# Kernel optimization log

Hardware: AMD Instinct MI355X
Metric: run time of the kernel (lower is better)

Reference implementation:

```python
import jax, jax.numpy as jnp
import numpy as np

H, F = 4, 32          # GAT heads, per-head channels (= hidden_dim)
NEG_ATT = 0.2         # GATConv attention leaky_relu slope (PyG default)
NEG_ACT = 0.01        # F.leaky_relu / nn.LeakyReLU default slope
NUM_ID = 9            # len(map_candid_to_numid)


def _leaky(x, s):
    return jnp.where(x >= 0, x, s * x)


def gat_conv(x, src, dst, n, W, att_src, att_dst, bias):
    # PyG GATConv(heads=4, concat=False): softmax over in-edges per dst node,
    # weighted scatter-add, mean over heads, then bias.
    h = (x @ W).reshape(n, H, F)
    a_s = jnp.einsum('nhf,hf->nh', h, att_src)
    a_d = jnp.einsum('nhf,hf->nh', h, att_dst)
    e = _leaky(a_s[src] + a_d[dst], NEG_ATT)                        # [E,H]
    m = jax.ops.segment_max(e, dst, num_segments=n)                 # stable softmax max
    m = jnp.where(jnp.isfinite(m), m, 0.0)
    ex = jnp.exp(e - m[dst])
    denom = jax.ops.segment_sum(ex, dst, num_segments=n) + 1e-16    # PyG softmax eps
    alpha = ex / denom[dst]
    out = jax.ops.segment_sum(alpha[:, :, None] * h[src], dst, num_segments=n)
    return out.mean(axis=1) + bias


def _gat_params(k, din):
    k1, k2, k3 = jax.random.split(k, 3)
    return (jax.random.normal(k1, (din, H * F), jnp.float32) * np.float32(1.0 / np.sqrt(din)),
            jax.random.normal(k2, (H, F), jnp.float32) * 0.1,
            jax.random.normal(k3, (H, F), jnp.float32) * 0.1,
            jnp.zeros((F,), jnp.float32))


def setup_inputs() -> dict:
    key = jax.random.key(0)
    ks = jax.random.split(key, 20)
    N, E, D = 100000, 800000, 3
    x = jax.random.normal(ks[0], (N, D), jnp.float32)
    x = x.at[: N // 2, 0].set(0.0)  # towers: x[:,0] == 0
    edge_index = jax.random.randint(ks[1], (2, E), 0, N, dtype=jnp.int64)
    edge_attr = jax.random.uniform(ks[2], (E, 1), dtype=jnp.float32)
    inp = {'x': x, 'edge_index': edge_index, 'edge_attr': edge_attr}
    for i, din in enumerate([D, F, F]):
        W, a_s, a_d, b = _gat_params(ks[3 + i], din)
        inp[f'W{i+1}'] = W; inp[f'a_src{i+1}'] = a_s
        inp[f'a_dst{i+1}'] = a_d; inp[f'b{i+1}'] = b
    mlp_dims = [(D + F, F), (F, F), (F, F), (F, F), (F, NUM_ID + 3)]
    for i, (di, do) in enumerate(mlp_dims):
        k1, k2 = jax.random.split(ks[10 + i])
        inp[f'mW{i+1}'] = jax.random.normal(k1, (di, do), jnp.float32) * np.float32(1.0 / np.sqrt(di))
        inp[f'mb{i+1}'] = jax.random.normal(k2, (do,), jnp.float32) * 0.01
    return inp


def reference(x, edge_index, edge_attr, W1, a_src1, a_dst1, b1,
              W2, a_src2, a_dst2, b2, W3, a_src3, a_dst3, b3,
              mW1, mb1, mW2, mb2, mW3, mb3, mW4, mb4, mW5, mb5):
    # edge_attr / batch are read but unused by the torch forward.
    n = x.shape[0]
    loops = jnp.arange(n, dtype=edge_index.dtype)  # add_self_loops=True
    src = jnp.concatenate([edge_index[0], loops])
    dst = jnp.concatenate([edge_index[1], loops])
    x1 = _leaky(gat_conv(x, src, dst, n, W1, a_src1, a_dst1, b1), NEG_ACT)
    x2 = _leaky(gat_conv(x1, src, dst, n, W2, a_src2, a_dst2, b2), NEG_ACT)
    x3 = _leaky(gat_conv(x2, src, dst, n, W3, a_src3, a_dst3, b3), NEG_ACT)
    h = jnp.concatenate([x, x3], axis=-1)
    for W, b in [(mW1, mb1), (mW2, mb2), (mW3, mb3), (mW4, mb4)]:
        h = _leaky(h @ W + b, NEG_ACT)  # Dropout(0.5) is identity in eval
    cands = h @ mW5 + mb5               # [N, 12]
    mask_tower = x[:, 0] == 0           # data-dependent split (eager-mode indexing)
    ct = cands[mask_tower]
    ck = cands[~mask_tower]
    return (ct[:, :NUM_ID], ck[:, :NUM_ID], ct[:, NUM_ID:], ck[:, NUM_ID:])
```

## Files before the change

kernel.cpp:

```cpp
#include <hip/hip_runtime.h>
#include <hip/hip_bf16.h>

#define DEV __device__ __forceinline__

DEV float bf2f(__hip_bfloat16 v) { return __bfloat162float(v); }

typedef unsigned long long ull;

__global__ void k_detect_zero(const unsigned short* xr, int nprobe, int* flag,
                              int* cnt, int N) {
    int i = blockIdx.x * 256 + threadIdx.x;
    if (i < N) cnt[i] = 0;
    if (blockIdx.x == 0) {
        __shared__ int red[256];
        int t = threadIdx.x, bad = 0;
        for (int j = t; j < nprobe; j += 256) {
            unsigned e = (xr[j] >> 7) & 0xFF;
            if (e >= 0x8F) bad++;
        }
        red[t] = bad; __syncthreads();
        for (int o = 128; o > 0; o >>= 1) { if (t < o) red[t] += red[t + o]; __syncthreads(); }
        if (t == 0) flag[0] = (red[0] > 256) ? 1 : 0;
    }
}

struct Seg  { const void* src; int off; int len; };
struct Segs { Seg s[22]; };

__global__ void k_fused(const void* xsrc, int nx3, Segs segs, float* canon,
                        const int* flag, const int* eidx, int E, int N,
                        int* cnt, int* msk, int* rank) {
    int f32 = flag[0];
    int t = threadIdx.x, b = blockIdx.x;
    if (b < 64) {
        for (int i = b * 256 + t; i < nx3; i += 64 * 256) {
            float v = f32 ? ((const float*)xsrc)[i] : bf2f(((const __hip_bfloat16*)xsrc)[i]);
            if (!(v == v) || fabsf(v) > 1e30f) v = 0.f;
            canon[i] = v;
            if (i % 3 == 0) msk[i / 3] = (v == 0.0f) ? 1 : 0;
        }
    } else if (b < 86) {
        Seg sg = segs.s[b - 64];
        for (int i = t; i < sg.len; i += 256) {
            float v = f32 ? ((const float*)sg.src)[i] : bf2f(((const __hip_bfloat16*)sg.src)[i]);
            if (!(v == v) || fabsf(v) > 1e30f) v = 0.f;
            canon[sg.off + i] = v;
        }
    } else {
        int e = (b - 86) * 256 + t;
        if (e < E) {
            int d = eidx[E + e];
            if ((unsigned)d < (unsigned)N) {
                int p = atomicAdd(&cnt[d], 1);
                rank[e] = p;
            }
        }
    }
}


DEV ull packval(const int* cnt, const int* msk, int i) {
    return ((ull)(unsigned)msk[i] << 32) | (unsigned)(cnt[i] + 1);
}

__global__ void k_scan_partial64(const int* __restrict__ cnt, const int* __restrict__ msk,
                                 int n, ull* __restrict__ partials) {
    __shared__ ull red[256];
    int t = threadIdx.x, b = blockIdx.x;
    int base = b * 1024 + t * 4;
    ull s = 0;
    #pragma unroll
    for (int j = 0; j < 4; j++) { int i = base + j; if (i < n) s += packval(cnt, msk, i); }
    red[t] = s; __syncthreads();
    for (int o = 128; o > 0; o >>= 1) { if (t < o) red[t] += red[t + o]; __syncthreads(); }
    if (t == 0) partials[b] = red[0];
}

__global__ void k_scan_final64(const int* __restrict__ cnt, int* __restrict__ msk, int n,
                               const ull* __restrict__ partials, int nb,
                               int* __restrict__ off, int* __restrict__ offN,
                               int* __restrict__ totals) {
    __shared__ ull sums[256];
    __shared__ ull redLT[256], redALL[256];
    int t = threadIdx.x, b = blockIdx.x;

    ull sLT = 0, sALL = 0;
    for (int i = t; i < nb; i += 256) {
        ull v = partials[i];
        sALL += v;
        if (i < b) sLT += v;
    }
    redLT[t] = sLT; redALL[t] = sALL; __syncthreads();
    for (int o = 128; o > 0; o >>= 1) {
        if (t < o) { redLT[t] += redLT[t + o]; redALL[t] += redALL[t + o]; }
        __syncthreads();
    }
    ull blockbase = redLT[0];
    if (b == 0 && t == 0) {
        ull tot = redALL[0];
        *offN = (int)(tot & 0xffffffffu);
        *totals = (int)(tot >> 32);
    }
    __syncthreads();

    int base = b * 1024 + t * 4;
    ull v0 = 0, v1 = 0, v2 = 0, v3 = 0;
    if (base     < n) v0 = packval(cnt, msk, base);
    if (base + 1 < n) v1 = packval(cnt, msk, base + 1);
    if (base + 2 < n) v2 = packval(cnt, msk, base + 2);
    if (base + 3 < n) v3 = packval(cnt, msk, base + 3);
    ull s = v0 + v1 + v2 + v3;
    sums[t] = s; __syncthreads();
    for (int o = 1; o < 256; o <<= 1) {
        ull x = (t >= o) ? sums[t - o] : 0;
        __syncthreads();
        sums[t] += x;
        __syncthreads();
    }
    ull run = blockbase + (sums[t] - s);
    #pragma unroll
    for (int j = 0; j < 4; j++) {
        int i = base + j;
        if (i < n) {
            off[i] = (int)(run & 0xffffffffu);
            msk[i] = (int)(run >> 32);
            run += (j == 0 ? v0 : j == 1 ? v1 : j == 2 ? v2 : v3);
        }
    }
}


__global__ __launch_bounds__(256) void k_fill_node1(
    const int* __restrict__ eidx, const int* __restrict__ rank, int E, int N,
    const int* __restrict__ off, int* __restrict__ esrc,
    const float* __restrict__ xF, const float* __restrict__ W,
    const float* __restrict__ atS, const float* __restrict__ atD,
    __hip_bfloat162* __restrict__ h2, float* __restrict__ as_, float* __restrict__ ad_,
    int gfill) {
    __shared__ float xl[64 * 4];
    int b = blockIdx.x;
    if (b < gfill) {
        int e = b * 256 + threadIdx.x;
        if (e < E) {
            int s = eidx[e], d = eidx[E + e];
            if ((unsigned)d < (unsigned)N && (unsigned)s < (unsigned)N)
                esrc[off[d] + rank[e]] = s;
        } else if (e < E + N) {
            int i = e - E;
            esrc[off[i + 1] - 1] = i;
        }
        return;
    }
    int t = threadIdx.x, lane = t & 63, w = t >> 6;
    int nblk = (b - gfill) * 64;
    int cnt = N - nblk; if (cnt > 64) cnt = 64;

    if (t < 64) xl[t * 4 + 3] = 0.f;
    for (int i = t; i < cnt * 3; i += 256) xl[(i / 3) * 4 + (i % 3)] = xF[(size_t)nblk * 3 + i];

    const float2* W2 = (const float2*)W;
    float2 Wr0 = W2[0 * 64 + lane], Wr1 = W2[1 * 64 + lane], Wr2 = W2[2 * 64 + lane];
    float2 aSp = ((const float2*)atS)[lane];
    float2 aDp = ((const float2*)atD)[lane];
    int hd = lane >> 4;
    __syncthreads();

    for (int i = 0; i < 16; i++) {
        int n = nblk + w * 16 + i;
        if (n >= N) break;
        float4 xv = ((const float4*)xl)[w * 16 + i];
        float acc0 = xv.x * Wr0.x + xv.y * Wr1.x + xv.z * Wr2.x;
        float acc1 = xv.x * Wr0.y + xv.y * Wr1.y + xv.z * Wr2.y;
        __hip_bfloat162 hv; hv.x = __float2bfloat16(acc0); hv.y = __float2bfloat16(acc1);
        h2[(size_t)n * 64 + lane] = hv;
        float p = acc0 * aSp.x + acc1 * aSp.y;
        float q = acc0 * aDp.x + acc1 * aDp.y;
        #pragma unroll
        for (int o = 1; o < 16; o <<= 1) { p += __shfl_xor(p, o, 64); q += __shfl_xor(q, o, 64); }
        if ((lane & 15) == 0) { as_[n * 4 + hd] = p; ad_[n * 4 + hd] = q; }
    }
}


__global__ __launch_bounds__(256) void k_node_mid(
    const float* __restrict__ xin, const float* __restrict__ W,
    const float* __restrict__ atS, const float* __restrict__ atD,
    int N, __hip_bfloat162* __restrict__ h2, float* __restrict__ as_, float* __restrict__ ad_) {
    __shared__ float xl[64 * 32];
    int t = threadIdx.x, lane = t & 63, w = t >> 6;
    int nblk = blockIdx.x * 64;
    int cnt = N - nblk; if (cnt > 64) cnt = 64;

    {
        const float4* g4 = (const float4*)(xin + (size_t)nblk * 32);
        float4* l4 = (float4*)xl;
        int lim = cnt * 8;
        if (t < lim) l4[t] = g4[t];
        int t2 = t + 256;
        if (t2 < lim) l4[t2] = g4[t2];
    }

    const float2* W2 = (const float2*)W;
    float2 Wr[32];
    #pragma unroll
    for (int k = 0; k < 32; k++) Wr[k] = W2[k * 64 + lane];
    float2 aSp = ((const float2*)atS)[lane];
    float2 aDp = ((const float2*)atD)[lane];
    int hd = lane >> 4;
    __syncthreads();

    for (int i = 0; i < 16; i++) {
        int n = nblk + w * 16 + i;
        if (n >= N) break;
        const float4* xv4 = (const float4*)&xl[(w * 16 + i) * 32];
        float acc0 = 0.f, acc1 = 0.f;
        #pragma unroll
        for (int kk = 0; kk < 8; kk++) {
            float4 xv = xv4[kk];
            acc0 += xv.x * Wr[4*kk+0].x; acc1 += xv.x * Wr[4*kk+0].y;
            acc0 += xv.y * Wr[4*kk+1].x; acc1 += xv.y * Wr[4*kk+1].y;
            acc0 += xv.z * Wr[4*kk+2].x; acc1 += xv.z * Wr[4*kk+2].y;
            acc0 += xv.w * Wr[4*kk+3].x; acc1 += xv.w * Wr[4*kk+3].y;
        }
        __hip_bfloat162 hv; hv.x = __float2bfloat16(acc0); hv.y = __float2bfloat16(acc1);
        h2[(size_t)n * 64 + lane] = hv;
        float p = acc0 * aSp.x + acc1 * aSp.y;
        float q = acc0 * aDp.x + acc1 * aDp.y;
        #pragma unroll
        for (int o = 1; o < 16; o <<= 1) { p += __shfl_xor(p, o, 64); q += __shfl_xor(q, o, 64); }
        if ((lane & 15) == 0) { as_[n * 4 + hd] = p; ad_[n * 4 + hd] = q; }
    }
}


constexpr int FCAP  = 64;
constexpr int FCAPP = 68;

__global__ __launch_bounds__(256) void k_edge(
    const __hip_bfloat162* __restrict__ h2, const float* __restrict__ as_,
    const float* __restrict__ ad_, const int* __restrict__ off,
    const int* __restrict__ esrc, const float* __restrict__ bias,
    int N, float* __restrict__ xout) {
    __shared__ float alphaS[4][4 * FCAPP];
    __shared__ int   srcS[4][FCAP];
    int t = threadIdx.x, lane = t & 63, w = t >> 6;
    int n = blockIdx.x * 4 + w;
    if (n >= N) return;
    int beg = off[n], end = off[n + 1];
    int deg = end - beg;
    float4 adn = ((const float4*)ad_)[n];
    const float4* as4 = (const float4*)as_;
    int hd = lane >> 4;

    float acc0 = 0.f, acc1 = 0.f;

    if (deg <= 16) {
        int e = lane >> 2, h = lane & 3;
        int s_e = n;
        float v = -1e30f;
        if (e < deg) {
            int s = esrc[beg + e];
            if ((unsigned)s < (unsigned)N) {
                s_e = s;
                float asv = as_[s * 4 + h];
                float adv = h == 0 ? adn.x : h == 1 ? adn.y : h == 2 ? adn.z : adn.w;
                v = asv + adv; v = v >= 0.f ? v : 0.2f * v;
            }
        }
        float m = v;
        #pragma unroll
        for (int o = 4; o < 64; o <<= 1) m = fmaxf(m, __shfl_xor(m, o, 64));
        float ex = (v > -1e29f) ? __expf(v - m) : 0.f;
        float ssum = ex;
        #pragma unroll
        for (int o = 4; o < 64; o <<= 1) ssum += __shfl_xor(ssum, o, 64);
        float inv = 1.f / (ssum + 1e-16f);
        float invH = __shfl(inv, hd, 64);

        #pragma unroll
        for (int c = 0; c < 4; c++) {
            if (4 * c < deg) {
                float w0 = __shfl(ex, 16 * c + 0  + hd, 64);
                float w1 = __shfl(ex, 16 * c + 4  + hd, 64);
                float w2 = __shfl(ex, 16 * c + 8  + hd, 64);
                float w3 = __shfl(ex, 16 * c + 12 + hd, 64);
                int s0 = __shfl(s_e, 16 * c + 0, 64);
                int s1 = __shfl(s_e, 16 * c + 4, 64);
                int s2 = __shfl(s_e, 16 * c + 8, 64);
                int s3 = __shfl(s_e, 16 * c + 12, 64);
                __hip_bfloat162 g0 = h2[(size_t)s0 * 64 + lane];
                __hip_bfloat162 g1 = h2[(size_t)s1 * 64 + lane];
                __hip_bfloat162 g2 = h2[(size_t)s2 * 64 + lane];
                __hip_bfloat162 g3 = h2[(size_t)s3 * 64 + lane];
                acc0 += w0 * bf2f(g0.x) + w1 * bf2f(g1.x) + w2 * bf2f(g2.x) + w3 * bf2f(g3.x);
                acc1 += w0 * bf2f(g0.y) + w1 * bf2f(g1.y) + w2 * bf2f(g2.y) + w3 * bf2f(g3.y);
            }
        }
        acc0 *= invH; acc1 *= invH;
    } else {
        bool fits = (deg <= FCAP);
        float m0 = -1e30f, m1 = -1e30f, m2 = -1e30f, m3 = -1e30f;
        for (int e = beg + lane; e < end; e += 64) {
            int s = esrc[e];
            if ((unsigned)s >= (unsigned)N) continue;
            float4 a = as4[s];
            float v0 = a.x + adn.x; v0 = v0 >= 0.f ? v0 : 0.2f * v0;
            float v1 = a.y + adn.y; v1 = v1 >= 0.f ? v1 : 0.2f * v1;
            float v2 = a.z + adn.z; v2 = v2 >= 0.f ? v2 : 0.2f * v2;
            float v3 = a.w + adn.w; v3 = v3 >= 0.f ? v3 : 0.2f * v3;
            m0 = fmaxf(m0, v0); m1 = fmaxf(m1, v1); m2 = fmaxf(m2, v2); m3 = fmaxf(m3, v3);
        }
        #pragma unroll
        for (int o = 1; o < 64; o <<= 1) {
            m0 = fmaxf(m0, __shfl_xor(m0, o, 64));
            m1 = fmaxf(m1, __shfl_xor(m1, o, 64));
            m2 = fmaxf(m2, __shfl_xor(m2, o, 64));
            m3 = fmaxf(m3, __shfl_xor(m3, o, 64));
        }
        float s0 = 0.f, s1 = 0.f, s2 = 0.f, s3 = 0.f;
        for (int e = beg + lane; e < end; e += 64) {
            int s = esrc[e];
            bool ok = (unsigned)s < (unsigned)N;
            float4 a = ok ? as4[s] : make_float4(-1e30f, -1e30f, -1e30f, -1e30f);
            float v0 = a.x + adn.x; v0 = v0 >= 0.f ? v0 : 0.2f * v0;
            float v1 = a.y + adn.y; v1 = v1 >= 0.f ? v1 : 0.2f * v1;
            float v2 = a.z + adn.z; v2 = v2 >= 0.f ? v2 : 0.2f * v2;
            float v3 = a.w + adn.w; v3 = v3 >= 0.f ? v3 : 0.2f * v3;
            float e0 = __expf(v0 - m0), e1 = __expf(v1 - m1);
            float e2 = __expf(v2 - m2), e3 = __expf(v3 - m3);
            s0 += e0; s1 += e1; s2 += e2; s3 += e3;
            if (fits) {
                int i = e - beg;
                srcS[w][i] = ok ? s : n;
                alphaS[w][0 * FCAPP + i] = e0;
                alphaS[w][1 * FCAPP + i] = e1;
                alphaS[w][2 * FCAPP + i] = e2;
                alphaS[w][3 * FCAPP + i] = e3;
            }
        }
        #pragma unroll
        for (int o = 1; o < 64; o <<= 1) {
            s0 += __shfl_xor(s0, o, 64); s1 += __shfl_xor(s1, o, 64);
            s2 += __shfl_xor(s2, o, 64); s3 += __shfl_xor(s3, o, 64);
        }
        float i0 = 1.f / (s0 + 1e-16f), i1 = 1.f / (s1 + 1e-16f);
        float i2 = 1.f / (s2 + 1e-16f), i3 = 1.f / (s3 + 1e-16f);
        float invH = hd == 0 ? i0 : hd == 1 ? i1 : hd == 2 ? i2 : i3;
        if (fits) {
            for (int i = 0; i < deg; i++) {
                int s = srcS[w][i];
                float wt = alphaS[w][hd * FCAPP + i];
                __hip_bfloat162 hv = h2[(size_t)s * 64 + lane];
                acc0 += wt * bf2f(hv.x);
                acc1 += wt * bf2f(hv.y);
            }
        } else {
            float mH  = hd == 0 ? m0 : hd == 1 ? m1 : hd == 2 ? m2 : m3;
            float adH = hd == 0 ? adn.x : hd == 1 ? adn.y : hd == 2 ? adn.z : adn.w;
            for (int e = beg; e < end; e++) {
                int s = esrc[e];
                if ((unsigned)s >= (unsigned)N) continue;
                float4 a = as4[s];
                float aH = hd == 0 ? a.x : hd == 1 ? a.y : hd == 2 ? a.z : a.w;
                float v = aH + adH; v = v >= 0.f ? v : 0.2f * v;
                float wt = __expf(v - mH);
                __hip_bfloat162 hv = h2[(size_t)s * 64 + lane];
                acc0 += wt * bf2f(hv.x);
                acc1 += wt * bf2f(hv.y);
            }
        }
        acc0 *= invH; acc1 *= invH;
    }
    acc0 += __shfl_xor(acc0, 16, 64); acc0 += __shfl_xor(acc0, 32, 64);
    acc1 += __shfl_xor(acc1, 16, 64); acc1 += __shfl_xor(acc1, 32, 64);
    if (lane < 16) {
        float o0 = acc0 * 0.25f + bias[2 * lane];     o0 = o0 >= 0.f ? o0 : 0.01f * o0;
        float o1 = acc1 * 0.25f + bias[2 * lane + 1]; o1 = o1 >= 0.f ? o1 : 0.01f * o1;
        ((float2*)xout)[(size_t)n * 16 + lane] = make_float2(o0, o1);
    }
}


__global__ __launch_bounds__(128) void k_mlp(
    const float* __restrict__ xF, const float* __restrict__ x3,
    const float* __restrict__ mW1, const float* __restrict__ mb1,
    const float* __restrict__ mW2, const float* __restrict__ mb2,
    const float* __restrict__ mW3, const float* __restrict__ mb3,
    const float* __restrict__ mW4, const float* __restrict__ mb4,
    const float* __restrict__ mW5, const float* __restrict__ mb5,
    const int* __restrict__ smask, const int* __restrict__ totals,
    const int* __restrict__ flag, int N, void* __restrict__ out) {
    __shared__ float W1[35 * 32], W2[1024], W3[1024], W4[1024], W5[32 * 12];
    __shared__ float B1[32], B2[32], B3[32], B4[32], B5[12];
    __shared__ float actA[35 * 128];
    __shared__ float actB[32 * 128];
    int t = threadIdx.x;
    for (int i = t; i < 1120; i += 128) W1[i] = mW1[i];
    for (int i = t; i < 1024; i += 128) { W2[i] = mW2[i]; W3[i] = mW3[i]; W4[i] = mW4[i]; }
    for (int i = t; i < 384; i += 128) W5[i] = mW5[i];
    if (t < 32) { B1[t] = mb1[t]; B2[t] = mb2[t]; B3[t] = mb3[t]; B4[t] = mb4[t]; }
    if (t < 12) B5[t] = mb5[t];
    __syncthreads();

    int n = blockIdx.x * 128 + t;
    bool alive = (n < N);
    float x0 = 0.f;
    if (alive) {
        x0 = xF[n * 3 + 0];
        actA[0 * 128 + t] = x0;
        actA[1 * 128 + t] = xF[n * 3 + 1];
        actA[2 * 128 + t] = xF[n * 3 + 2];
        for (int i = 0; i < 32; i++) actA[(3 + i) * 128 + t] = x3[(size_t)n * 32 + i];
    }

    float acc[32];

    #pragma unroll
    for (int o = 0; o < 32; o++) acc[o] = B1[o];
    #pragma unroll 2
    for (int i = 0; i < 35; i++) {
        float ai = actA[i * 128 + t];
        const float4* w4 = (const float4*)&W1[i * 32];
        #pragma unroll
        for (int q = 0; q < 8; q++) {
            float4 w = w4[q];
            acc[q*4+0] += ai * w.x; acc[q*4+1] += ai * w.y;
            acc[q*4+2] += ai * w.z; acc[q*4+3] += ai * w.w;
        }
    }
    #pragma unroll
    for (int o = 0; o < 32; o++) { float v = acc[o]; actB[o * 128 + t] = (v >= 0.f ? v : 0.01f * v); }

    #pragma unroll
    for (int o = 0; o < 32; o++) acc[o] = B2[o];
    #pragma unroll 2
    for (int i = 0; i < 32; i++) {
        float ai = actB[i * 128 + t];
        const float4* w4 = (const float4*)&W2[i * 32];
        #pragma unroll
        for (int q = 0; q < 8; q++) {
            float4 w = w4[q];
            acc[q*4+0] += ai * w.x; acc[q*4+1] += ai * w.y;
            acc[q*4+2] += ai * w.z; acc[q*4+3] += ai * w.w;
        }
    }
    #pragma unroll
    for (int o = 0; o < 32; o++) { float v = acc[o]; actA[o * 128 + t] = (v >= 0.f ? v : 0.01f * v); }

    #pragma unroll
    for (int o = 0; o < 32; o++) acc[o] = B3[o];
    #pragma unroll 2
    for (int i = 0; i < 32; i++) {
        float ai = actA[i * 128 + t];
        const float4* w4 = (const float4*)&W3[i * 32];
        #pragma unroll
        for (int q = 0; q < 8; q++) {
            float4 w = w4[q];
            acc[q*4+0] += ai * w.x; acc[q*4+1] += ai * w.y;
            acc[q*4+2] += ai * w.z; acc[q*4+3] += ai * w.w;
        }
    }
    #pragma unroll
    for (int o = 0; o < 32; o++) { float v = acc[o]; actB[o * 128 + t] = (v >= 0.f ? v : 0.01f * v); }

    #pragma unroll
    for (int o = 0; o < 32; o++) acc[o] = B4[o];
    #pragma unroll 2
    for (int i = 0; i < 32; i++) {
        float ai = actB[i * 128 + t];
        const float4* w4 = (const float4*)&W4[i * 32];
        #pragma unroll
        for (int q = 0; q < 8; q++) {
            float4 w = w4[q];
            acc[q*4+0] += ai * w.x; acc[q*4+1] += ai * w.y;
            acc[q*4+2] += ai * w.z; acc[q*4+3] += ai * w.w;
        }
    }
    #pragma unroll
    for (int o = 0; o < 32; o++) { float v = acc[o]; actA[o * 128 + t] = (v >= 0.f ? v : 0.01f * v); }

    float d[12];
    #pragma unroll
    for (int o = 0; o < 12; o++) d[o] = B5[o];
    #pragma unroll 2
    for (int i = 0; i < 32; i++) {
        float ai = actA[i * 128 + t];
        const float4* w4 = (const float4*)&W5[i * 12];
        #pragma unroll
        for (int q = 0; q < 3; q++) {
            float4 w = w4[q];
            d[q*4+0] += ai * w.x; d[q*4+1] += ai * w.y;
            d[q*4+2] += ai * w.z; d[q*4+3] += ai * w.w;
        }
    }
    if (!alive) return;
    #pragma unroll
    for (int o = 0; o < 12; o++) if (!(d[o] == d[o])) d[o] = 0.f;

    bool tower = (x0 == 0.0f);
    int r = smask[n];
    int Nt = *totals;
    int f32o = *flag;
    int base9, base3, rr;
    if (tower) { rr = r;     base9 = 0;      base3 = 9 * N; }
    else       { rr = n - r; base9 = 9 * Nt; base3 = 9 * N + 3 * Nt; }
    if (f32o) {
        float* o = (float*)out;
        #pragma unroll
        for (int j = 0; j < 9; j++) o[base9 + rr * 9 + j] = d[j];
        #pragma unroll
        for (int j = 0; j < 3; j++) o[base3 + rr * 3 + j] = d[9 + j];
    } else {
        __hip_bfloat16* o = (__hip_bfloat16*)out;
        #pragma unroll
        for (int j = 0; j < 9; j++) o[base9 + rr * 9 + j] = __float2bfloat16(d[j]);
        #pragma unroll
        for (int j = 0; j < 3; j++) o[base3 + rr * 3 + j] = __float2bfloat16(d[9 + j]);
    }
}


extern "C" void kernel_launch(void* const* d_in, const int* in_sizes, int n_in,
                              void* d_out, int out_size, void* d_ws, size_t ws_size,
                              hipStream_t stream) {
    const void* xraw = d_in[0];
    const int*  eidx = (const int*)d_in[1];

    int N  = in_sizes[0] / 3;
    int E  = in_sizes[1] / 2;
    int EE = E + N;

    Segs segs;
    int coff[22];
    int canonN = 3 * N;
    for (int i = 3; i <= 24; i++) {
        int a = i - 3;
        segs.s[a].src = d_in[i];
        segs.s[a].off = canonN;
        segs.s[a].len = in_sizes[i];
        coff[a] = canonN;
        canonN += in_sizes[i];
    }

    auto alignv = [](size_t v, size_t a) { return (v + a - 1) & ~(a - 1); };
    char* base = (char*)d_ws;
    size_t o = 0;
    float* canon = (float*)(base + o); o = alignv(o + (size_t)canonN * 4, 16);
    int* flag     = (int*)(base + o); o = alignv(o + 16, 16);
    ull* partials = (ull*)(base + o); o = alignv(o + 1024 * 8, 16);
    int* totals   = (int*)(base + o); o = alignv(o + 16, 16);
    int* off      = (int*)(base + o); o = alignv(o + (size_t)(N + 1) * 4, 16);
    int* cnt      = (int*)(base + o); o = alignv(o + (size_t)N * 4, 16);
    int* esrc     = (int*)(base + o); o = alignv(o + (size_t)EE * 4, 16);
    int* rank     = (int*)(base + o); o = alignv(o + (size_t)E * 4, 16);
    int* msk      = (int*)(base + o); o = alignv(o + (size_t)N * 4, 256);
    __hip_bfloat162* h2 = (__hip_bfloat162*)(base + o); o = alignv(o + (size_t)N * 64 * 4, 16);
    float* xb  = (float*)(base + o); o = alignv(o + (size_t)N * 32 * 4, 16);
    float* as_ = (float*)(base + o); o = alignv(o + (size_t)N * 16, 16);
    float* ad_ = (float*)(base + o);

    int nb = (N + 1023) / 1024;
    int gN = (N + 255) / 256;
    int g4 = (N + 3) / 4;
    int g64 = (N + 63) / 64;
    int gM = (N + 127) / 128;
    int gfill = (EE + 255) / 256;

    int nprobe = in_sizes[0] < 4096 ? in_sizes[0] : 4096;
    k_detect_zero<<<gN, 256, 0, stream>>>((const unsigned short*)xraw, nprobe, flag, cnt, N);
    k_fused<<<86 + (E + 255) / 256, 256, 0, stream>>>(xraw, 3 * N, segs, canon, flag,
                                                      eidx, E, N, cnt, msk, rank);
    k_scan_partial64<<<nb, 256, 0, stream>>>(cnt, msk, N, partials);
    k_scan_final64<<<nb, 256, 0, stream>>>(cnt, msk, N, partials, nb, off, off + N, totals);

    float* xF = canon;
    const float* W1  = canon + coff[0];  const float* aS1 = canon + coff[1];
    const float* aD1 = canon + coff[2];  const float* b1  = canon + coff[3];
    const float* W2  = canon + coff[4];  const float* aS2 = canon + coff[5];
    const float* aD2 = canon + coff[6];  const float* b2  = canon + coff[7];
    const float* W3  = canon + coff[8];  const float* aS3 = canon + coff[9];
    const float* aD3 = canon + coff[10]; const float* b3  = canon + coff[11];

    k_fill_node1<<<gfill + g64, 256, 0, stream>>>(eidx, rank, E, N, off, esrc,
                                                  xF, W1, aS1, aD1, h2, as_, ad_, gfill);
    k_edge<<<g4, 256, 0, stream>>>(h2, as_, ad_, off, esrc, b1, N, xb);
    k_node_mid<<<g64, 256, 0, stream>>>(xb, W2, aS2, aD2, N, h2, as_, ad_);
    k_edge<<<g4, 256, 0, stream>>>(h2, as_, ad_, off, esrc, b2, N, xb);
    k_node_mid<<<g64, 256, 0, stream>>>(xb, W3, aS3, aD3, N, h2, as_, ad_);
    k_edge<<<g4, 256, 0, stream>>>(h2, as_, ad_, off, esrc, b3, N, xb);

    k_mlp<<<gM, 128, 0, stream>>>(xF, xb,
        canon + coff[12], canon + coff[13], canon + coff[14], canon + coff[15],
        canon + coff[16], canon + coff[17], canon + coff[18], canon + coff[19],
        canon + coff[20], canon + coff[21], msk, totals, flag, N, d_out);
}
```

Before: 436.3 us.

## Fold dtype detection into fused prep kernel and stage edge weights in LDS

Removes the separate detection kernel. Every block of the fused prep kernel now probes the input dtype itself, and cnt is zeroed with an async memset. In the low-degree path of the edge kernel, the softmax weights and source indices go into shared memory and are read back as float4/int4 vectors instead of through many cross-lane shuffles. The cost is that every block of the large fused grid now does the redundant 4096-element probe and reduction, which adds work and global reads per block.

Measured after the change: 437.3 us. No clear change (+0.2%).

```diff
diff --git a/kernel.cpp b/kernel.cpp
--- a/kernel.cpp
+++ b/kernel.cpp
@@ -7,31 +7,25 @@
 
 typedef unsigned long long ull;
 
-__global__ void k_detect_zero(const unsigned short* xr, int nprobe, int* flag,
-                              int* cnt, int N) {
-    int i = blockIdx.x * 256 + threadIdx.x;
-    if (i < N) cnt[i] = 0;
-    if (blockIdx.x == 0) {
-        __shared__ int red[256];
-        int t = threadIdx.x, bad = 0;
-        for (int j = t; j < nprobe; j += 256) {
-            unsigned e = (xr[j] >> 7) & 0xFF;
-            if (e >= 0x8F) bad++;
-        }
-        red[t] = bad; __syncthreads();
-        for (int o = 128; o > 0; o >>= 1) { if (t < o) red[t] += red[t + o]; __syncthreads(); }
-        if (t == 0) flag[0] = (red[0] > 256) ? 1 : 0;
-    }
-}
-
 struct Seg  { const void* src; int off; int len; };
 struct Segs { Seg s[22]; };
 
-__global__ void k_fused(const void* xsrc, int nx3, Segs segs, float* canon,
-                        const int* flag, const int* eidx, int E, int N,
+__global__ void k_fused(const void* xsrc, int nx3, int nprobe, Segs segs,
+                        float* canon, int* flag, const int* eidx, int E, int N,
                         int* cnt, int* msk, int* rank) {
-    int f32 = flag[0];
+    __shared__ int red[256];
     int t = threadIdx.x, b = blockIdx.x;
+    const unsigned short* xr = (const unsigned short*)xsrc;
+    int bad = 0;
+    for (int j = t; j < nprobe; j += 256) {
+        unsigned e = (xr[j] >> 7) & 0xFF;
+        if (e >= 0x8F) bad++;
+    }
+    red[t] = bad; __syncthreads();
+    for (int o = 128; o > 0; o >>= 1) { if (t < o) red[t] += red[t + o]; __syncthreads(); }
+    int f32 = (red[0] > 256) ? 1 : 0;
+    if (b == 0 && t == 0) flag[0] = f32;
+
     if (b < 64) {
         for (int i = b * 256 + t; i < nx3; i += 64 * 256) {
             float v = f32 ? ((const float*)xsrc)[i] : bf2f(((const __hip_bfloat16*)xsrc)[i]);
@@ -241,8 +235,8 @@
     const float* __restrict__ ad_, const int* __restrict__ off,
     const int* __restrict__ esrc, const float* __restrict__ bias,
     int N, float* __restrict__ xout) {
-    __shared__ float alphaS[4][4 * FCAPP];
-    __shared__ int   srcS[4][FCAP];
+    __shared__ __align__(16) float alphaS[4][4 * FCAPP];
+    __shared__ __align__(16) int   srcS[4][FCAP];
     int t = threadIdx.x, lane = t & 63, w = t >> 6;
     int n = blockIdx.x * 4 + w;
     if (n >= N) return;
@@ -277,23 +271,22 @@
         float inv = 1.f / (ssum + 1e-16f);
         float invH = __shfl(inv, hd, 64);
 
+        alphaS[w][h * 20 + e] = ex;
+        if (h == 0) srcS[w][e] = s_e;
+
         #pragma unroll
         for (int c = 0; c < 4; c++) {
             if (4 * c < deg) {
-                float w0 = __shfl(ex, 16 * c + 0  + hd, 64);
-                float w1 = __shfl(ex, 16 * c + 4  + hd, 64);
-                float w2 = __shfl(ex, 16 * c + 8  + hd, 64);
-                float w3 = __shfl(ex, 16 * c + 12 + hd, 64);
-                int s0 = __shfl(s_e, 16 * c + 0, 64);
-                int s1 = __shfl(s_e, 16 * c + 4, 64);
-                int s2 = __shfl(s_e, 16 * c + 8, 64);
-                int s3 = __shfl(s_e, 16 * c + 12, 64);
-                __hip_bfloat162 g0 = h2[(size_t)s0 * 64 + lane];
-                __hip_bfloat162 g1 = h2[(size_t)s1 * 64 + lane];
-                __hip_bfloat162 g2 = h2[(size_t)s2 * 64 + lane];
-                __hip_bfloat162 g3 = h2[(size_t)s3 * 64 + lane];
-                acc0 += w0 * bf2f(g0.x) + w1 * bf2f(g1.x) + w2 * bf2f(g2.x) + w3 * bf2f(g3.x);
-                acc1 += w0 * bf2f(g0.y) + w1 * bf2f(g1.y) + w2 * bf2f(g2.y) + w3 * bf2f(g3.y);
+                float4 wt4 = *(const float4*)&alphaS[w][hd * 20 + 4 * c];
+                int4   s4  = *(const int4*)&srcS[w][4 * c];
+                __hip_bfloat162 g0 = h2[(size_t)s4.x * 64 + lane];
+                __hip_bfloat162 g1 = h2[(size_t)s4.y * 64 + lane];
+                __hip_bfloat162 g2 = h2[(size_t)s4.z * 64 + lane];
+                __hip_bfloat162 g3 = h2[(size_t)s4.w * 64 + lane];
+                acc0 += wt4.x * bf2f(g0.x) + wt4.y * bf2f(g1.x)
+                      + wt4.z * bf2f(g2.x) + wt4.w * bf2f(g3.x);
+                acc1 += wt4.x * bf2f(g0.y) + wt4.y * bf2f(g1.y)
+                      + wt4.z * bf2f(g2.y) + wt4.w * bf2f(g3.y);
             }
         }
         acc0 *= invH; acc1 *= invH;
@@ -560,16 +553,15 @@
     float* ad_ = (float*)(base + o);
 
     int nb = (N + 1023) / 1024;
-    int gN = (N + 255) / 256;
     int g4 = (N + 3) / 4;
     int g64 = (N + 63) / 64;
     int gM = (N + 127) / 128;
     int gfill = (EE + 255) / 256;
 
     int nprobe = in_sizes[0] < 4096 ? in_sizes[0] : 4096;
-    k_detect_zero<<<gN, 256, 0, stream>>>((const unsigned short*)xraw, nprobe, flag, cnt, N);
-    k_fused<<<86 + (E + 255) / 256, 256, 0, stream>>>(xraw, 3 * N, segs, canon, flag,
-                                                      eidx, E, N, cnt, msk, rank);
+    hipMemsetAsync(cnt, 0, (size_t)N * 4, stream);
+    k_fused<<<86 + (E + 255) / 256, 256, 0, stream>>>(xraw, 3 * N, nprobe, segs, canon,
+                                                      flag, eidx, E, N, cnt, msk, rank);
     k_scan_partial64<<<nb, 256, 0, stream>>>(cnt, msk, N, partials);
     k_scan_final64<<<nb, 256, 0, stream>>>(cnt, msk, N, partials, nb, off, off + N, totals);
 
```
